# Performance work log

Hardware: AMD Instinct MI355X
Metric: run time of the kernel (lower is better)

## Reference

```python
import jax, jax.numpy as jnp
import numpy as np

HIDDEN = 4096
N_HEADS = 32
N_KV = 8
HEAD_DIM = 128
THETA = 1000000.0
EPS = 1e-6


def setup_inputs() -> dict:
    key = jax.random.key(0)
    ks = jax.random.split(key, 8)
    B, T = 2, 2048
    s_in = 1.0 / np.sqrt(HIDDEN)
    s_o = 1.0 / np.sqrt(N_HEADS * HEAD_DIM)
    return {
        "x": jax.random.normal(ks[0], (B, T, HIDDEN), dtype=jnp.float32),
        "wq": jax.random.normal(ks[1], (HIDDEN, N_HEADS * HEAD_DIM), dtype=jnp.float32) * s_in,
        "wk": jax.random.normal(ks[2], (HIDDEN, N_KV * HEAD_DIM), dtype=jnp.float32) * s_in,
        "wv": jax.random.normal(ks[3], (HIDDEN, N_KV * HEAD_DIM), dtype=jnp.float32) * s_in,
        "wo": jax.random.normal(ks[4], (N_HEADS * HEAD_DIM, HIDDEN), dtype=jnp.float32) * s_o,
        "q_norm_w": jax.random.normal(ks[5], (HEAD_DIM,), dtype=jnp.float32) * 0.02 + 1.0,
        "k_norm_w": jax.random.normal(ks[6], (HEAD_DIM,), dtype=jnp.float32) * 0.02 + 1.0,
    }


def _rms_norm(x, w):
    rms = jnp.sqrt(jnp.mean(x * x, axis=-1, keepdims=True) + EPS)
    return w * x / rms


def _apply_rope(inputs, position_ids):
    # inputs: [B, T, H, D]; position_ids: [B, T]
    fraction = 2 * jnp.arange(0, HEAD_DIM // 2, dtype=jnp.float32) / HEAD_DIM
    timescale = jnp.power(THETA, fraction)  # [D/2]
    x = (position_ids[..., None] / timescale[None, None, :])[..., None, :]  # [B,T,1,D/2]
    sin, cos = jnp.sin(x), jnp.cos(x)
    a, b = jnp.split(inputs, 2, axis=-1)
    return jnp.concatenate([a * cos - b * sin, b * cos + a * sin], axis=-1).astype(inputs.dtype)


def reference(x, wq, wk, wv, wo, q_norm_w, k_norm_w):
    B, T, _ = x.shape
    q = _rms_norm((x @ wq).reshape(B, T, N_HEADS, HEAD_DIM), q_norm_w)
    k = _rms_norm((x @ wk).reshape(B, T, N_KV, HEAD_DIM), k_norm_w)
    v = (x @ wv).reshape(B, T, N_KV, HEAD_DIM)

    position_ids = jnp.broadcast_to(jnp.arange(T)[None, :], (B, T))
    q = _apply_rope(q, position_ids)
    k = _apply_rope(k, position_ids)

    # GQA repeat of k/v to match query heads
    num_groups = N_HEADS // N_KV
    k = jnp.repeat(k, num_groups, axis=2)  # [B,T,H,D]
    v = jnp.repeat(v, num_groups, axis=2)

    scale = 1.0 / np.sqrt(HEAD_DIM)
    scores = jnp.einsum("bqhd,bkhd->bhqk", q, k) * scale  # [B,H,T,T]
    causal = jnp.tril(jnp.ones((T, T), dtype=bool))
    scores = jnp.where(causal[None, None, :, :], scores, jnp.finfo(scores.dtype).min)
    probs = jax.nn.softmax(scores, axis=-1)
    attn = jnp.einsum("bhqk,bkhd->bqhd", probs, v)  # [B,T,H,D]

    return attn.reshape(B, T, N_HEADS * HEAD_DIM) @ wo
```

## Files before the change

kernel.cpp:

```cpp
#include <hip/hip_runtime.h>
#include <hip/hip_bf16.h>
#include <math.h>

#define HID 4096
#define DH  128
#define NQH 32
#define NKVH 8
#define BB  2
#define TQ  2048
#define BT  (BB*TQ)

typedef __bf16 bf16x8 __attribute__((ext_vector_type(8)));
typedef __bf16 bf16x4 __attribute__((ext_vector_type(4)));
typedef float  f32x4  __attribute__((ext_vector_type(4)));
typedef float  f32x16 __attribute__((ext_vector_type(16)));

#define MFMA(a,b,c)   __builtin_amdgcn_mfma_f32_16x16x32_bf16(a,b,c,0,0,0)
#define MFMA32(a,b,c) __builtin_amdgcn_mfma_f32_32x32x16_bf16(a,b,c,0,0,0)

__device__ __forceinline__ void gl_lds16(const void* g, void* l) {
    __builtin_amdgcn_global_load_lds(
        (const __attribute__((address_space(1))) unsigned int*)g,
        (__attribute__((address_space(3))) unsigned int*)l, 16, 0, 0);
}

__global__ __launch_bounds__(256) void conv_kernel(
    const float* __restrict__ x, __bf16* __restrict__ xb)
{
    const size_t i = (((size_t)blockIdx.x << 8) + threadIdx.x) << 3;
    const f32x4 f0 = *(const f32x4*)(x + i);
    const f32x4 f1 = *(const f32x4*)(x + i + 4);
    bf16x8 o;
    #pragma unroll
    for (int j = 0; j < 4; ++j) { o[j] = (__bf16)f0[j]; o[j + 4] = (__bf16)f1[j]; }
    *(bf16x8*)(xb + i) = o;
}

__global__ __launch_bounds__(256,3) void qkv_kernel(
    const __bf16* __restrict__ xb, const float* __restrict__ wq,
    const float* __restrict__ wk,  const float* __restrict__ wv,
    const float* __restrict__ qnw, const float* __restrict__ knw,
    __bf16* __restrict__ qb, __bf16* __restrict__ kb, __bf16* __restrict__ vt)
{
    __shared__ union {
        struct { __bf16 A[128*64]; float B[64*128]; } s;
        float Ct[64][132];
    } u;

    const int bid = blockIdx.x;
    const int wg  = (bid & 7) * 192 + (bid >> 3);
    const int ct  = wg >> 5;
    const int rt  = wg & 31;
    const int tid = threadIdx.x;
    const int lane = tid & 63;
    const int wave = tid >> 6;
    const int wr = wave >> 1, wc = wave & 1;
    const int l31 = lane & 31, hi = lane >> 5;

    const float* W; int Ncols, kind, hsel;
    if (ct < NQH)            { W = wq; Ncols = NQH*DH;  hsel = ct;          kind = 0; }
    else if (ct < NQH+NKVH)  { W = wk; Ncols = NKVH*DH; hsel = ct-NQH;      kind = 1; }
    else                     { W = wv; Ncols = NKVH*DH; hsel = ct-NQH-NKVH; kind = 2; }
    const int col0 = hsel * DH;
    const int row0 = rt << 7;

    const int arow = (wave << 5) + (lane >> 3);
    const int acol = (((lane & 7) ^ ((lane >> 3) & 7)) << 3);
    const __bf16* aSrc = xb + (size_t)(row0 + arow) * HID + acol;

    const int bk  = (wave << 4) + (lane >> 5);
    const int bn  = (lane & 31) << 2;
    const float* bSrc = W + (size_t)bk * Ncols + col0 + bn;

    const int aBase0 = ((wr << 6) + l31) << 6;
    const int aBase1 = aBase0 + (32 << 6);
    const int axor   = l31 & 7;
    const int bCol   = (wc << 6) + l31;

    f32x16 acc00 = {0.f,0.f,0.f,0.f,0.f,0.f,0.f,0.f,0.f,0.f,0.f,0.f,0.f,0.f,0.f,0.f};
    f32x16 acc01 = acc00, acc10 = acc00, acc11 = acc00;

    for (int k0 = 0; k0 < HID; k0 += 64) {
        __syncthreads();
        #pragma unroll
        for (int i = 0; i < 4; ++i)
            gl_lds16(aSrc + k0 + (size_t)(i << 3) * HID,
                     &u.s.A[((wave << 5) + (i << 3)) << 6]);
        #pragma unroll
        for (int i = 0; i < 8; ++i)
            gl_lds16(bSrc + (size_t)(k0 + (i << 1)) * Ncols,
                     &u.s.B[((wave << 4) + (i << 1)) << 7]);
        __syncthreads();

        #pragma unroll
        for (int kr = 0; kr < 4; ++kr) {
            const int ag = (((kr << 1) + hi) ^ axor) << 3;
            bf16x8 fa0 = *(const bf16x8*)&u.s.A[aBase0 + ag];
            bf16x8 fa1 = *(const bf16x8*)&u.s.A[aBase1 + ag];
            const int kb8 = (kr << 4) + (hi << 3);
            bf16x8 fb0, fb1;
            #pragma unroll
            for (int j = 0; j < 8; ++j) {
                fb0[j] = (__bf16)u.s.B[((kb8 + j) << 7) + bCol];
                fb1[j] = (__bf16)u.s.B[((kb8 + j) << 7) + bCol + 32];
            }
            acc00 = MFMA32(fa0, fb0, acc00);
            acc01 = MFMA32(fa0, fb1, acc01);
            acc10 = MFMA32(fa1, fb0, acc10);
            acc11 = MFMA32(fa1, fb1, acc11);
        }
    }

    const int bidx = row0 >> 11;
    #pragma unroll
    for (int pass = 0; pass < 2; ++pass) {
        __syncthreads();
        if (wr == pass) {
            #pragma unroll
            for (int rc = 0; rc < 4; ++rc) {
                const f32x16 a = (rc == 0) ? acc00 : (rc == 1) ? acc01
                               : (rc == 2) ? acc10 : acc11;
                const int rr = (rc >> 1), cc = (rc & 1);
                #pragma unroll
                for (int r = 0; r < 16; ++r) {
                    const int row = (rr << 5) + (r & 3) + ((r >> 2) << 3) + (hi << 2);
                    u.Ct[row][(wc << 6) + (cc << 5) + l31] = a[r];
                }
            }
        }
        __syncthreads();
        if (kind == 2) {
            const int d  = tid >> 1;
            const int t0 = (tid & 1) << 5;
            __bf16* dst = vt + ((size_t)(bidx*NKVH + hsel)*DH + d)*TQ
                             + (row0 & (TQ-1)) + (pass << 6) + t0;
            #pragma unroll
            for (int c = 0; c < 8; ++c) {
                bf16x4 o;
                #pragma unroll
                for (int i = 0; i < 4; ++i) o[i] = (__bf16)u.Ct[t0 + (c << 2) + i][d];
                *(bf16x4*)(dst + (c << 2)) = o;
            }
        } else {
            const int r  = tid >> 2;
            const int c0 = (tid & 3) << 5;
            float ss = 0.f;
            #pragma unroll
            for (int i = 0; i < 32; ++i) { const float v = u.Ct[r][c0 + i]; ss += v*v; }
            ss += __shfl_xor(ss, 1); ss += __shfl_xor(ss, 2);
            const float inv = rsqrtf(ss * (1.0f/DH) + 1e-6f);
            const float* nw = kind ? knw : qnw;
            const int tpos = (row0 & (TQ-1)) + (pass << 6) + r;
            __bf16* dst = (kind == 0)
                ? qb + ((size_t)(bidx*NQH  + hsel)*TQ + tpos)*DH + c0
                : kb + ((size_t)(bidx*NKVH + hsel)*TQ + tpos)*DH + c0;
            #pragma unroll
            for (int cc = 0; cc < 8; ++cc) {
                bf16x4 o;
                #pragma unroll
                for (int i = 0; i < 4; ++i) {
                    const int c = c0 + (cc << 2) + i;
                    const float nv = nw[c]      * u.Ct[r][c]      * inv;
                    const float pv = nw[c ^ 64] * u.Ct[r][c ^ 64] * inv;
                    const float ang = (float)tpos * exp2f(-0.31143075895f * (float)(c & 63));
                    float sn, cs; sincosf(ang, &sn, &cs);
                    o[i] = (__bf16)((c < 64) ? (nv*cs - pv*sn) : (nv*cs + pv*sn));
                }
                *(bf16x4*)(dst + (cc << 2)) = o;
            }
        }
    }
}

__global__ __launch_bounds__(64) void attn_kernel(
    const __bf16* __restrict__ qb, const __bf16* __restrict__ kb,
    const __bf16* __restrict__ vt, __bf16* __restrict__ ab)
{
    const int qt = blockIdx.x;
    const int bh = blockIdx.y;
    const int b = bh >> 5, h = bh & 31, hk = h >> 2;
    const int lane = threadIdx.x;
    const int m16 = lane & 15, quad = lane >> 4;

    const __bf16* qp = qb + (size_t)(b*NQH  + h )*TQ*DH;
    const __bf16* kp = kb + (size_t)(b*NKVH + hk)*TQ*DH;
    const __bf16* vp = vt + (size_t)(b*NKVH + hk)*DH*TQ;

    const int q0 = qt << 4;
    bf16x8 aq[4];
    #pragma unroll
    for (int ks = 0; ks < 4; ++ks)
        aq[ks] = *(const bf16x8*)(qp + (size_t)(q0 + m16)*DH + (ks << 5) + (quad << 3));

    f32x4 o[8];
    #pragma unroll
    for (int cc = 0; cc < 8; ++cc) o[cc] = (f32x4){0.f,0.f,0.f,0.f};
    float mrow[4] = {-1e30f,-1e30f,-1e30f,-1e30f};
    float lrow[4] = {0.f,0.f,0.f,0.f};

    __shared__ alignas(16) __bf16 Pl[16][40];
    const float scale = 0.08838834764831845f;

    const int ktmax = (q0 + 15) >> 5;
    for (int kt = 0; kt <= ktmax; ++kt) {
        const int k0 = kt << 5;
        f32x4 s0 = {0.f,0.f,0.f,0.f}, s1 = {0.f,0.f,0.f,0.f};
        #pragma unroll
        for (int ks = 0; ks < 4; ++ks) {
            bf16x8 b0 = *(const bf16x8*)(kp + (size_t)(k0 + m16)*DH      + (ks << 5) + (quad << 3));
            bf16x8 b1 = *(const bf16x8*)(kp + (size_t)(k0 + 16 + m16)*DH + (ks << 5) + (quad << 3));
            s0 = MFMA(aq[ks], b0, s0);
            s1 = MFMA(aq[ks], b1, s1);
        }
        float alpha[4];
        #pragma unroll
        for (int r = 0; r < 4; ++r) {
            const int qg = q0 + (quad << 2) + r;
            const int kg = k0 + m16;
            float a_ = (kg      <= qg) ? s0[r]*scale : -1e30f;
            float b_ = (kg + 16 <= qg) ? s1[r]*scale : -1e30f;
            float t = fmaxf(a_, b_);
            t = fmaxf(t, __shfl_xor(t, 1)); t = fmaxf(t, __shfl_xor(t, 2));
            t = fmaxf(t, __shfl_xor(t, 4)); t = fmaxf(t, __shfl_xor(t, 8));
            const float mn = fmaxf(mrow[r], t);
            alpha[r] = __expf(mrow[r] - mn);
            const float p0 = __expf(a_ - mn);
            const float p1 = __expf(b_ - mn);
            float rs = p0 + p1;
            rs += __shfl_xor(rs, 1); rs += __shfl_xor(rs, 2);
            rs += __shfl_xor(rs, 4); rs += __shfl_xor(rs, 8);
            lrow[r] = lrow[r]*alpha[r] + rs;
            mrow[r] = mn;
            Pl[(quad << 2) + r][m16]      = (__bf16)p0;
            Pl[(quad << 2) + r][m16 + 16] = (__bf16)p1;
        }
        __syncthreads();
        const bf16x8 pf = *(const bf16x8*)&Pl[m16][quad << 3];
        #pragma unroll
        for (int cc = 0; cc < 8; ++cc) {
            #pragma unroll
            for (int r = 0; r < 4; ++r) o[cc][r] *= alpha[r];
            bf16x8 vf = *(const bf16x8*)(vp + (size_t)((cc << 4) + m16)*TQ + k0 + (quad << 3));
            o[cc] = MFMA(pf, vf, o[cc]);
        }
        __syncthreads();
    }

    #pragma unroll
    for (int r = 0; r < 4; ++r) {
        const int t = q0 + (quad << 2) + r;
        const float invl = 1.0f / lrow[r];
        __bf16* dst = ab + (size_t)(b*TQ + t)*(NQH*DH) + h*DH + m16;
        #pragma unroll
        for (int cc = 0; cc < 8; ++cc)
            dst[cc << 4] = (__bf16)(o[cc][r] * invl);
    }
}

__global__ __launch_bounds__(256,3) void ogemm_kernel(
    const __bf16* __restrict__ Am, const float* __restrict__ W,
    float* __restrict__ out)
{
    __shared__ struct { __bf16 A[128*64]; float B[64*128]; } s;

    const int bid = blockIdx.x;
    const int wg  = (bid & 7) * 128 + (bid >> 3);
    const int ct  = wg >> 5, rt = wg & 31;
    const int tid = threadIdx.x;
    const int lane = tid & 63;
    const int wave = tid >> 6;
    const int wr = wave >> 1, wc = wave & 1;
    const int l31 = lane & 31, hi = lane >> 5;
    const int col0 = ct << 7;
    const int row0 = rt << 7;

    const int arow = (wave << 5) + (lane >> 3);
    const int acol = (((lane & 7) ^ ((lane >> 3) & 7)) << 3);
    const __bf16* aSrc = Am + (size_t)(row0 + arow) * HID + acol;

    const int bk  = (wave << 4) + (lane >> 5);
    const int bn  = (lane & 31) << 2;
    const float* bSrc = W + (size_t)bk * HID + col0 + bn;

    const int aBase0 = ((wr << 6) + l31) << 6;
    const int aBase1 = aBase0 + (32 << 6);
    const int axor   = l31 & 7;
    const int bCol   = (wc << 6) + l31;

    f32x16 acc00 = {0.f,0.f,0.f,0.f,0.f,0.f,0.f,0.f,0.f,0.f,0.f,0.f,0.f,0.f,0.f,0.f};
    f32x16 acc01 = acc00, acc10 = acc00, acc11 = acc00;

    for (int k0 = 0; k0 < HID; k0 += 64) {
        __syncthreads();
        #pragma unroll
        for (int i = 0; i < 4; ++i)
            gl_lds16(aSrc + k0 + (size_t)(i << 3) * HID,
                     &s.A[((wave << 5) + (i << 3)) << 6]);
        #pragma unroll
        for (int i = 0; i < 8; ++i)
            gl_lds16(bSrc + (size_t)(k0 + (i << 1)) * HID,
                     &s.B[((wave << 4) + (i << 1)) << 7]);
        __syncthreads();

        #pragma unroll
        for (int kr = 0; kr < 4; ++kr) {
            const int ag = (((kr << 1) + hi) ^ axor) << 3;
            bf16x8 fa0 = *(const bf16x8*)&s.A[aBase0 + ag];
            bf16x8 fa1 = *(const bf16x8*)&s.A[aBase1 + ag];
            const int kb8 = (kr << 4) + (hi << 3);
            bf16x8 fb0, fb1;
            #pragma unroll
            for (int j = 0; j < 8; ++j) {
                fb0[j] = (__bf16)s.B[((kb8 + j) << 7) + bCol];
                fb1[j] = (__bf16)s.B[((kb8 + j) << 7) + bCol + 32];
            }
            acc00 = MFMA32(fa0, fb0, acc00);
            acc01 = MFMA32(fa0, fb1, acc01);
            acc10 = MFMA32(fa1, fb0, acc10);
            acc11 = MFMA32(fa1, fb1, acc11);
        }
    }

    #pragma unroll
    for (int rc = 0; rc < 4; ++rc) {
        const f32x16 a = (rc == 0) ? acc00 : (rc == 1) ? acc01
                       : (rc == 2) ? acc10 : acc11;
        const int rr = (rc >> 1), cc = (rc & 1);
        #pragma unroll
        for (int r = 0; r < 16; ++r) {
            const int row = row0 + (wr << 6) + (rr << 5)
                          + (r & 3) + ((r >> 2) << 3) + (hi << 2);
            out[(size_t)row * HID + col0 + (wc << 6) + (cc << 5) + l31] = a[r];
        }
    }
}

extern "C" void kernel_launch(void* const* d_in, const int* in_sizes, int n_in,
                              void* d_out, int out_size, void* d_ws, size_t ws_size,
                              hipStream_t stream)
{
    const float* x   = (const float*)d_in[0];
    const float* wq  = (const float*)d_in[1];
    const float* wk  = (const float*)d_in[2];
    const float* wv  = (const float*)d_in[3];
    const float* wo  = (const float*)d_in[4];
    const float* qnw = (const float*)d_in[5];
    const float* knw = (const float*)d_in[6];
    float* out = (float*)d_out;

    __bf16* qb = (__bf16*)d_out;
    __bf16* xb = (__bf16*)d_out + (size_t)BB*NQH*TQ*DH;
    __bf16* kb = (__bf16*)d_ws;
    __bf16* vt = kb + (size_t)BB*NKVH*TQ*DH;
    __bf16* ab = vt + (size_t)BB*NKVH*TQ*DH;
    const size_t need = ((size_t)BB*NKVH*TQ*DH*2 + (size_t)BB*TQ*NQH*DH)*sizeof(__bf16);
    if (ws_size < need) return;

    conv_kernel<<<dim3((BT*HID)/2048), 256, 0, stream>>>(x, xb);
    qkv_kernel<<<dim3(48*32), 256, 0, stream>>>(xb, wq, wk, wv, qnw, knw, qb, kb, vt);
    attn_kernel<<<dim3(TQ/16, BB*NQH), 64, 0, stream>>>(qb, kb, vt, ab);
    ogemm_kernel<<<dim3(32*32), 256, 0, stream>>>(ab, wo, out);
}
```

Baseline: 1.491 ms.

## Pack four attention waves per block and use lazy softmax rescaling

The attention kernel now runs four independent 64-thread waves per 256-thread block, each with its own LDS tile for P, and swaps the block barriers for an lgkmcnt wait. The online softmax only rescales the running max and the output accumulators when some row's new max exceeds the old one by more than 8, and the per-row sum is kept per lane and reduced once at the end. This removes per-tile shuffle reductions, exp work and accumulator rescales, and makes the launch coarser. In exchange, probabilities can reach up to e^8 before rescaling, which risks bf16 precision in P, and waves in one block do unequal causal work.

```diff
diff --git a/kernel.cpp b/kernel.cpp
--- a/kernel.cpp
+++ b/kernel.cpp
@@ -172,14 +172,16 @@
     }
 }
 
-__global__ __launch_bounds__(64) void attn_kernel(
+__global__ __launch_bounds__(256) void attn_kernel(
     const __bf16* __restrict__ qb, const __bf16* __restrict__ kb,
     const __bf16* __restrict__ vt, __bf16* __restrict__ ab)
 {
-    const int qt = blockIdx.x;
+    const int tid  = threadIdx.x;
+    const int wave = tid >> 6;
+    const int lane = tid & 63;
+    const int qt = (blockIdx.x << 2) + wave;
     const int bh = blockIdx.y;
     const int b = bh >> 5, h = bh & 31, hk = h >> 2;
-    const int lane = threadIdx.x;
     const int m16 = lane & 15, quad = lane >> 4;
 
     const __bf16* qp = qb + (size_t)(b*NQH  + h )*TQ*DH;
@@ -196,9 +198,9 @@
     #pragma unroll
     for (int cc = 0; cc < 8; ++cc) o[cc] = (f32x4){0.f,0.f,0.f,0.f};
     float mrow[4] = {-1e30f,-1e30f,-1e30f,-1e30f};
-    float lrow[4] = {0.f,0.f,0.f,0.f};
-
-    __shared__ alignas(16) __bf16 Pl[16][40];
+    float lsum[4] = {0.f,0.f,0.f,0.f};
+
+    __shared__ alignas(16) __bf16 Pl[4][16][40];
     const float scale = 0.08838834764831845f;
 
     const int ktmax = (q0 + 15) >> 5;
@@ -212,44 +214,54 @@
             s0 = MFMA(aq[ks], b0, s0);
             s1 = MFMA(aq[ks], b1, s1);
         }
-        float alpha[4];
+        float a_[4], b_[4];
+        bool need = false;
         #pragma unroll
         for (int r = 0; r < 4; ++r) {
             const int qg = q0 + (quad << 2) + r;
             const int kg = k0 + m16;
-            float a_ = (kg      <= qg) ? s0[r]*scale : -1e30f;
-            float b_ = (kg + 16 <= qg) ? s1[r]*scale : -1e30f;
-            float t = fmaxf(a_, b_);
-            t = fmaxf(t, __shfl_xor(t, 1)); t = fmaxf(t, __shfl_xor(t, 2));
-            t = fmaxf(t, __shfl_xor(t, 4)); t = fmaxf(t, __shfl_xor(t, 8));
-            const float mn = fmaxf(mrow[r], t);
-            alpha[r] = __expf(mrow[r] - mn);
-            const float p0 = __expf(a_ - mn);
-            const float p1 = __expf(b_ - mn);
-            float rs = p0 + p1;
-            rs += __shfl_xor(rs, 1); rs += __shfl_xor(rs, 2);
-            rs += __shfl_xor(rs, 4); rs += __shfl_xor(rs, 8);
-            lrow[r] = lrow[r]*alpha[r] + rs;
-            mrow[r] = mn;
-            Pl[(quad << 2) + r][m16]      = (__bf16)p0;
-            Pl[(quad << 2) + r][m16 + 16] = (__bf16)p1;
-        }
-        __syncthreads();
-        const bf16x8 pf = *(const bf16x8*)&Pl[m16][quad << 3];
+            a_[r] = (kg      <= qg) ? s0[r]*scale : -1e30f;
+            b_[r] = (kg + 16 <= qg) ? s1[r]*scale : -1e30f;
+            need |= (fmaxf(a_[r], b_[r]) > mrow[r] + 8.0f);
+        }
+        if (__any(need)) {
+            #pragma unroll
+            for (int r = 0; r < 4; ++r) {
+                float t = fmaxf(a_[r], b_[r]);
+                t = fmaxf(t, __shfl_xor(t, 1)); t = fmaxf(t, __shfl_xor(t, 2));
+                t = fmaxf(t, __shfl_xor(t, 4)); t = fmaxf(t, __shfl_xor(t, 8));
+                const float mn = fmaxf(mrow[r], t);
+                const float al = __expf(mrow[r] - mn);
+                lsum[r] *= al;
+                mrow[r] = mn;
+                #pragma unroll
+                for (int cc = 0; cc < 8; ++cc) o[cc][r] *= al;
+            }
+        }
+        #pragma unroll
+        for (int r = 0; r < 4; ++r) {
+            const float p0 = __expf(a_[r] - mrow[r]);
+            const float p1 = __expf(b_[r] - mrow[r]);
+            lsum[r] += p0 + p1;
+            Pl[wave][(quad << 2) + r][m16]      = (__bf16)p0;
+            Pl[wave][(quad << 2) + r][m16 + 16] = (__bf16)p1;
+        }
+        asm volatile("s_waitcnt lgkmcnt(0)" ::: "memory");
+        const bf16x8 pf = *(const bf16x8*)&Pl[wave][m16][quad << 3];
         #pragma unroll
         for (int cc = 0; cc < 8; ++cc) {
-            #pragma unroll
-            for (int r = 0; r < 4; ++r) o[cc][r] *= alpha[r];
             bf16x8 vf = *(const bf16x8*)(vp + (size_t)((cc << 4) + m16)*TQ + k0 + (quad << 3));
             o[cc] = MFMA(pf, vf, o[cc]);
         }
-        __syncthreads();
     }
 
     #pragma unroll
     for (int r = 0; r < 4; ++r) {
+        float ls = lsum[r];
+        ls += __shfl_xor(ls, 1); ls += __shfl_xor(ls, 2);
+        ls += __shfl_xor(ls, 4); ls += __shfl_xor(ls, 8);
+        const float invl = 1.0f / ls;
         const int t = q0 + (quad << 2) + r;
-        const float invl = 1.0f / lrow[r];
         __bf16* dst = ab + (size_t)(b*TQ + t)*(NQH*DH) + h*DH + m16;
         #pragma unroll
         for (int cc = 0; cc < 8; ++cc)
@@ -358,6 +370,6 @@
 
     conv_kernel<<<dim3((BT*HID)/2048), 256, 0, stream>>>(x, xb);
     qkv_kernel<<<dim3(48*32), 256, 0, stream>>>(xb, wq, wk, wv, qnw, knw, qb, kb, vt);
-    attn_kernel<<<dim3(TQ/16, BB*NQH), 64, 0, stream>>>(qb, kb, vt, ab);
+    attn_kernel<<<dim3(TQ/64, BB*NQH), 256, 0, stream>>>(qb, kb, vt, ab);
     ogemm_kernel<<<dim3(32*32), 256, 0, stream>>>(ab, wo, out);
 }
```

After: 1.732 ms. 16.1% more time.
